# Kernel optimization log

Hardware: AMD Instinct MI355X
Metric: run time of the kernel (lower is better)

The kernel has to match this reference:

```python
import jax, jax.numpy as jnp
import numpy as np

N = 20480      # total nodes
E = 327680     # total edges (avg degree 16)
B = 16         # graphs in batch
IN = 16        # node feature dim
H = 8          # hidden_out_channel
CO = 64        # conv_out_channel
ET = 36        # n_edge_types
EF = 2         # edge_features
OUT = 1        # classifier out
DIMS = [(IN, H), (H, H), (H, H), (H, CO)]


def setup_inputs() -> dict:
    key = jax.random.key(0)
    ks = jax.random.split(key, 32)
    inp = {}
    inp['x'] = jax.random.normal(ks[0], (N, IN), jnp.float32)
    inp['edge_index'] = jax.random.randint(ks[1], (2, E), 0, N)
    inp['edge_type'] = jax.random.randint(ks[2], (E,), 0, ET)
    inp['edge_attr'] = jax.random.normal(ks[3], (E, EF), jnp.float32)
    inp['cell_type'] = jax.random.randint(ks[4], (N,), 0, 2)
    inp['batch'] = (jnp.arange(N) // (N // B)).astype(jnp.int32)
    i = 5
    for l, (ci, co) in enumerate(DIMS, 1):
        d = ci * co
        s = 1.0 / np.sqrt(EF)
        inp[f'emb{l}'] = jax.random.normal(ks[i], (ET, d), jnp.float32) * 0.02; i += 1
        inp[f'wh{l}'] = jax.random.normal(ks[i], (EF, d), jnp.float32) * s; i += 1
        inp[f'bh{l}'] = jnp.zeros((d,), jnp.float32)
        inp[f'wg{l}'] = jax.random.normal(ks[i], (EF, d), jnp.float32) * s; i += 1
        inp[f'bg{l}'] = jnp.zeros((d,), jnp.float32)
        inp[f'root{l}'] = jax.random.normal(ks[i], (ci, co), jnp.float32) / np.sqrt(ci); i += 1
        inp[f'bias{l}'] = jnp.zeros((co,), jnp.float32)
    inp['clf_w'] = jax.random.normal(ks[i], (CO, OUT), jnp.float32) / np.sqrt(CO)
    inp['clf_b'] = jnp.zeros((OUT,), jnp.float32)
    return inp


def edge_weights(etype, ef, emb, wh, bh, wg, bg):
    # EdgeNN: relu(embedding(type) * fc_h(feat) + fc_g(feat)) -> [E, cin*cout]
    return jax.nn.relu(emb[etype] * (ef @ wh + bh) + (ef @ wg + bg))


def nnconv(h, src, dst, W, root, bias):
    # NNConv(aggr='mean', root_weight=True): gather src feats, per-edge matmul, scatter-mean
    cin, cout = root.shape
    msg = jnp.einsum('ei,eio->eo', h[src], W.reshape(-1, cin, cout))  # [E, cout]
    agg = jax.ops.segment_sum(msg, dst, num_segments=N)
    deg = jax.ops.segment_sum(jnp.ones_like(msg[:, 0]), dst, num_segments=N)
    return agg / jnp.maximum(deg, 1.0)[:, None] + h @ root + bias


def reference(x, edge_index, edge_type, edge_attr, cell_type, batch,
              emb1, wh1, bh1, wg1, bg1, root1, bias1,
              emb2, wh2, bh2, wg2, bg2, root2, bias2,
              emb3, wh3, bh3, wg3, bg3, root3, bias3,
              emb4, wh4, bh4, wg4, bg4, root4, bias4,
              clf_w, clf_b):
    src, dst = edge_index[0], edge_index[1]
    layers = [(emb1, wh1, bh1, wg1, bg1, root1, bias1),
              (emb2, wh2, bh2, wg2, bg2, root2, bias2),
              (emb3, wh3, bh3, wg3, bg3, root3, bias3),
              (emb4, wh4, bh4, wg4, bg4, root4, bias4)]
    h = x
    for (emb, wh, bh, wg, bg, root, bias) in layers:  # fixed 4 structurally-distinct layers
        W = edge_weights(edge_type, edge_attr, emb, wh, bh, wg, bg)
        h = jax.nn.relu(nnconv(h, src, dst, W, root, bias))
    # gated scatter-mean pooling over tumor cells (cell_type == 1)
    gate = (cell_type == 1).astype(jnp.int32)
    seg = gate * (batch.astype(jnp.int32) + 1)  # 0 = masked-out bucket
    pooled = jax.ops.segment_sum(h, seg, num_segments=B + 1)
    cnt = jax.ops.segment_sum(jnp.ones((h.shape[0],), h.dtype), seg, num_segments=B + 1)
    pooled = (pooled / jnp.maximum(cnt, 1.0)[:, None])[1:B + 1]  # [B, CO]
    return jax.nn.sigmoid(pooled @ clf_w + clf_b)  # hazards [B, OUT]
```

## Files before the change

### kernel.cpp

```cpp
#include <hip/hip_runtime.h>
#include <math.h>

#define NN 20480
#define NE 327680
#define NBATCH 16

typedef float v2f __attribute__((ext_vector_type(2)));

#if __has_builtin(__builtin_elementwise_max)
#define VMAX0(a) __builtin_elementwise_max((a), (v2f){0.f, 0.f})
#else
static __device__ __forceinline__ v2f VMAX0(v2f a) {
  v2f r; r.x = fmaxf(a.x, 0.f); r.y = fmaxf(a.y, 0.f); return r;
}
#endif

__global__ void hist_kernel(const int* __restrict__ dst, int* __restrict__ cnt) {
  int e = blockIdx.x * blockDim.x + threadIdx.x;
  if (e < NE) atomicAdd(&cnt[dst[e]], 1);
}

__global__ __launch_bounds__(1024) void scan_kernel(const int* __restrict__ cnt,
                                                    int* __restrict__ off,
                                                    int* __restrict__ cur) {
  __shared__ int part[1024];
  int tid = threadIdx.x;
  const int PT = NN / 1024;
  int loc[PT];
  int run = 0;
  int base = tid * PT;
#pragma unroll
  for (int k = 0; k < PT; k++) { loc[k] = run; run += cnt[base + k]; }
  part[tid] = run;
  __syncthreads();
  for (int d = 1; d < 1024; d <<= 1) {
    int t = (tid >= d) ? part[tid - d] : 0;
    __syncthreads();
    part[tid] += t;
    __syncthreads();
  }
  int pre = (tid == 0) ? 0 : part[tid - 1];
#pragma unroll
  for (int k = 0; k < PT; k++) {
    off[base + k] = pre + loc[k];
    cur[base + k] = pre + loc[k];
  }
  if (tid == 1023) off[NN] = pre + run;
}

__global__ void scatter_kernel(const int* __restrict__ src, const int* __restrict__ dst,
                               const int* __restrict__ etype, const float* __restrict__ eattr,
                               int* __restrict__ cur, float4* __restrict__ es) {
  int e = blockIdx.x * blockDim.x + threadIdx.x;
  if (e >= NE) return;
  int d = dst[e];
  int pos = atomicAdd(&cur[d], 1);
  es[pos] = make_float4(__int_as_float(src[e]), __int_as_float(etype[e]),
                        eattr[2 * e], eattr[2 * e + 1]);
}

__global__ __launch_bounds__(256) void layer_small16(
    const int* __restrict__ off, const float4* __restrict__ es,
    const float* __restrict__ h_in,
    const float* __restrict__ emb, const float* __restrict__ wh,
    const float* __restrict__ bh, const float* __restrict__ wg,
    const float* __restrict__ bg,
    const float* __restrict__ root, const float* __restrict__ bias,
    float* __restrict__ h_out) {
  constexpr int D = 128;
  constexpr int S = D + 1;
  __shared__ float semb[36 * S];
  for (int idx = threadIdx.x; idx < 36 * D; idx += 256) {
    int t = idx / D, io = idx - t * D;
    semb[t * S + io] = emb[idx];
  }
  int lane = threadIdx.x & 63;
  int o = lane & 7;
  int ihalf = (lane >> 3) & 1;
  int esub = lane >> 4;
  int ibase = ihalf * 8;
  v2f rwh0[4], rwh1[4], rbh[4], rwg0[4], rwg1[4], rbg[4], rroot[4];
#pragma unroll
  for (int p = 0; p < 4; p++) {
    int a = (ibase + 2 * p) * 8 + o, b = (ibase + 2 * p + 1) * 8 + o;
    rwh0[p] = (v2f){wh[a], wh[b]};
    rwh1[p] = (v2f){wh[D + a], wh[D + b]};
    rbh[p]  = (v2f){bh[a], bh[b]};
    rwg0[p] = (v2f){wg[a], wg[b]};
    rwg1[p] = (v2f){wg[D + a], wg[D + b]};
    rbg[p]  = (v2f){bg[a], bg[b]};
    rroot[p] = (v2f){root[a], root[b]};
  }
  float rbias = bias[o];
  __syncthreads();
  int wid = __builtin_amdgcn_readfirstlane(blockIdx.x * 4 + (threadIdx.x >> 6));
  for (int k = 0; k < 2; k++) {
    int n = wid * 2 + k;
    int beg = off[n], end = off[n + 1];
    float acc = 0.f;
    for (int j = beg + esub; j < end; j += 4) {
      float4 rec = es[j];
      int s = __float_as_int(rec.x);
      int t = __float_as_int(rec.y);
      v2f ef0 = (v2f){rec.z, rec.z}, ef1 = (v2f){rec.w, rec.w};
      const float4* hp = (const float4*)(h_in + s * 16 + ibase);
      float4 h0 = hp[0], h1 = hp[1];
      v2f hv[4] = {(v2f){h0.x, h0.y}, (v2f){h0.z, h0.w},
                   (v2f){h1.x, h1.y}, (v2f){h1.z, h1.w}};
      const float* st = &semb[t * S + ibase * 8 + o];
      v2f msg = {0.f, 0.f};
#pragma unroll
      for (int p = 0; p < 4; p++) {
        v2f hval = ef0 * rwh0[p] + ef1 * rwh1[p] + rbh[p];
        v2f gval = ef0 * rwg0[p] + ef1 * rwg1[p] + rbg[p];
        v2f stv = (v2f){st[(2 * p) * 8], st[(2 * p + 1) * 8]};
        msg += hv[p] * VMAX0(stv * hval + gval);
      }
      acc += msg.x + msg.y;
    }
    acc += __shfl_xor(acc, 8);
    acc += __shfl_xor(acc, 16);
    acc += __shfl_xor(acc, 32);
    const float* hn = h_in + n * 16 + ibase;
    v2f rtv = {0.f, 0.f};
#pragma unroll
    for (int p = 0; p < 4; p++)
      rtv += (v2f){hn[2 * p], hn[2 * p + 1]} * rroot[p];
    float rt = rtv.x + rtv.y;
    rt += __shfl_xor(rt, 8);
    float deg = (float)(end - beg);
    float val = fmaxf(rbias + rt + acc / fmaxf(deg, 1.f), 0.f);
    if (lane < 8) h_out[n * 8 + o] = val;
  }
}

__global__ __launch_bounds__(256) void layer_small8(
    const int* __restrict__ off, const float4* __restrict__ es,
    const float* __restrict__ h_in,
    const float* __restrict__ emb, const float* __restrict__ wh,
    const float* __restrict__ bh, const float* __restrict__ wg,
    const float* __restrict__ bg,
    const float* __restrict__ root, const float* __restrict__ bias,
    float* __restrict__ h_out) {
  constexpr int D = 64;
  constexpr int S = D + 1;
  __shared__ float semb[36 * S];
  for (int idx = threadIdx.x; idx < 36 * D; idx += 256) {
    int t = idx / D, io = idx - t * D;
    semb[t * S + io] = emb[idx];
  }
  int lane = threadIdx.x & 63;
  int o = lane & 7, esub = lane >> 3;
  v2f rwh0[4], rwh1[4], rbh[4], rwg0[4], rwg1[4], rbg[4], rroot[4];
#pragma unroll
  for (int p = 0; p < 4; p++) {
    int a = (2 * p) * 8 + o, b = (2 * p + 1) * 8 + o;
    rwh0[p] = (v2f){wh[a], wh[b]};
    rwh1[p] = (v2f){wh[D + a], wh[D + b]};
    rbh[p]  = (v2f){bh[a], bh[b]};
    rwg0[p] = (v2f){wg[a], wg[b]};
    rwg1[p] = (v2f){wg[D + a], wg[D + b]};
    rbg[p]  = (v2f){bg[a], bg[b]};
    rroot[p] = (v2f){root[a], root[b]};
  }
  float rbias = bias[o];
  __syncthreads();
  int wid = __builtin_amdgcn_readfirstlane(blockIdx.x * 4 + (threadIdx.x >> 6));
  for (int k = 0; k < 4; k++) {
    int n = wid * 4 + k;
    int beg = off[n], end = off[n + 1];
    float acc = 0.f;
    for (int j = beg + esub; j < end; j += 8) {
      float4 rec = es[j];
      int s = __float_as_int(rec.x);
      int t = __float_as_int(rec.y);
      v2f ef0 = (v2f){rec.z, rec.z}, ef1 = (v2f){rec.w, rec.w};
      const float4* hp = (const float4*)(h_in + s * 8);
      float4 h0 = hp[0], h1 = hp[1];
      v2f hv[4] = {(v2f){h0.x, h0.y}, (v2f){h0.z, h0.w},
                   (v2f){h1.x, h1.y}, (v2f){h1.z, h1.w}};
      const float* st = &semb[t * S + o];
      v2f msg = {0.f, 0.f};
#pragma unroll
      for (int p = 0; p < 4; p++) {
        v2f hval = ef0 * rwh0[p] + ef1 * rwh1[p] + rbh[p];
        v2f gval = ef0 * rwg0[p] + ef1 * rwg1[p] + rbg[p];
        v2f stv = (v2f){st[(2 * p) * 8], st[(2 * p + 1) * 8]};
        msg += hv[p] * VMAX0(stv * hval + gval);
      }
      acc += msg.x + msg.y;
    }
    acc += __shfl_xor(acc, 8);
    acc += __shfl_xor(acc, 16);
    acc += __shfl_xor(acc, 32);
    float deg = (float)(end - beg);
    const float* hn = h_in + n * 8;
    v2f rtv = {0.f, 0.f};
#pragma unroll
    for (int p = 0; p < 4; p++)
      rtv += (v2f){hn[2 * p], hn[2 * p + 1]} * rroot[p];
    float val = fmaxf(rbias + rtv.x + rtv.y + acc / fmaxf(deg, 1.f), 0.f);
    if (lane < 8) h_out[n * 8 + o] = val;
  }
}

__global__ __launch_bounds__(256) void layer_l4(
    const int* __restrict__ off, const float4* __restrict__ es,
    const float* __restrict__ h_in,
    const float* __restrict__ emb, const float* __restrict__ wh,
    const float* __restrict__ bh, const float* __restrict__ wg,
    const float* __restrict__ bg,
    const float* __restrict__ root, const float* __restrict__ bias,
    float* __restrict__ h_out) {
  int lane = threadIdx.x & 63;
  v2f rwh0[4], rwh1[4], rbh[4], rwg0[4], rwg1[4], rbg[4], rroot[4];
#pragma unroll
  for (int p = 0; p < 4; p++) {
    int a = (2 * p) * 64 + lane, b = (2 * p + 1) * 64 + lane;
    rwh0[p] = (v2f){wh[a], wh[b]};
    rwh1[p] = (v2f){wh[512 + a], wh[512 + b]};
    rbh[p]  = (v2f){bh[a], bh[b]};
    rwg0[p] = (v2f){wg[a], wg[b]};
    rwg1[p] = (v2f){wg[512 + a], wg[512 + b]};
    rbg[p]  = (v2f){bg[a], bg[b]};
    rroot[p] = (v2f){root[a], root[b]};
  }
  float rbias = bias[lane];
  int n = __builtin_amdgcn_readfirstlane(blockIdx.x * 4 + (threadIdx.x >> 6));
  int beg = off[n], end = off[n + 1];
  float acc0 = 0.f, acc1 = 0.f;
  int e = beg;
  for (; e + 2 <= end; e += 2) {
    float4 r0 = es[e], r1 = es[e + 1];
    int s0 = __float_as_int(r0.x), t0 = __float_as_int(r0.y);
    int s1 = __float_as_int(r1.x), t1 = __float_as_int(r1.y);
    const float4* hp0 = (const float4*)(h_in + s0 * 8);
    const float4* hp1 = (const float4*)(h_in + s1 * 8);
    float4 a0 = hp0[0], a1 = hp0[1];
    float4 b0 = hp1[0], b1 = hp1[1];
    const float* st0 = emb + t0 * 512 + lane;
    const float* st1 = emb + t1 * 512 + lane;
    v2f sv0[4], sv1[4];
#pragma unroll
    for (int p = 0; p < 4; p++) sv0[p] = (v2f){st0[(2 * p) * 64], st0[(2 * p + 1) * 64]};
#pragma unroll
    for (int p = 0; p < 4; p++) sv1[p] = (v2f){st1[(2 * p) * 64], st1[(2 * p + 1) * 64]};
    v2f hva[4] = {(v2f){a0.x, a0.y}, (v2f){a0.z, a0.w},
                  (v2f){a1.x, a1.y}, (v2f){a1.z, a1.w}};
    v2f hvb[4] = {(v2f){b0.x, b0.y}, (v2f){b0.z, b0.w},
                  (v2f){b1.x, b1.y}, (v2f){b1.z, b1.w}};
    v2f e00 = (v2f){r0.z, r0.z}, e01 = (v2f){r0.w, r0.w};
    v2f e10 = (v2f){r1.z, r1.z}, e11 = (v2f){r1.w, r1.w};
    v2f m0 = {0.f, 0.f}, m1 = {0.f, 0.f};
#pragma unroll
    for (int p = 0; p < 4; p++) {
      v2f hv0 = e00 * rwh0[p] + e01 * rwh1[p] + rbh[p];
      v2f gv0 = e00 * rwg0[p] + e01 * rwg1[p] + rbg[p];
      m0 += hva[p] * VMAX0(sv0[p] * hv0 + gv0);
      v2f hv1 = e10 * rwh0[p] + e11 * rwh1[p] + rbh[p];
      v2f gv1 = e10 * rwg0[p] + e11 * rwg1[p] + rbg[p];
      m1 += hvb[p] * VMAX0(sv1[p] * hv1 + gv1);
    }
    acc0 += m0.x + m0.y;
    acc1 += m1.x + m1.y;
  }
  if (e < end) {
    float4 r0 = es[e];
    int s0 = __float_as_int(r0.x), t0 = __float_as_int(r0.y);
    const float4* hp0 = (const float4*)(h_in + s0 * 8);
    float4 a0 = hp0[0], a1 = hp0[1];
    const float* st0 = emb + t0 * 512 + lane;
    v2f hva[4] = {(v2f){a0.x, a0.y}, (v2f){a0.z, a0.w},
                  (v2f){a1.x, a1.y}, (v2f){a1.z, a1.w}};
    v2f e00 = (v2f){r0.z, r0.z}, e01 = (v2f){r0.w, r0.w};
    v2f m0 = {0.f, 0.f};
#pragma unroll
    for (int p = 0; p < 4; p++) {
      v2f hv0 = e00 * rwh0[p] + e01 * rwh1[p] + rbh[p];
      v2f gv0 = e00 * rwg0[p] + e01 * rwg1[p] + rbg[p];
      v2f stv = (v2f){st0[(2 * p) * 64], st0[(2 * p + 1) * 64]};
      m0 += hva[p] * VMAX0(stv * hv0 + gv0);
    }
    acc0 += m0.x + m0.y;
  }
  float acc = acc0 + acc1;
  float deg = (float)(end - beg);
  const float* hn = h_in + n * 8;
  v2f rtv = {0.f, 0.f};
#pragma unroll
  for (int p = 0; p < 4; p++)
    rtv += (v2f){hn[2 * p], hn[2 * p + 1]} * rroot[p];
  h_out[n * 64 + lane] = fmaxf(rbias + rtv.x + rtv.y + acc / fmaxf(deg, 1.f), 0.f);
}

__global__ __launch_bounds__(256) void pool1_kernel(
    const float* __restrict__ h4, const int* __restrict__ ct,
    float* __restrict__ pooled, float* __restrict__ pcnt) {
  __shared__ float ss[4][64];
  __shared__ float sc[4];
  int b = blockIdx.x / 20, c = blockIdx.x % 20;
  int base = b * (NN / NBATCH) + c * 64;
  int o = threadIdx.x & 63, sub = threadIdx.x >> 6;
  float sum = 0.f, cnt = 0.f;
  for (int j = sub; j < 64; j += 4) {
    int n = base + j;
    if (ct[n] == 1) { sum += h4[n * 64 + o]; cnt += 1.f; }
  }
  ss[sub][o] = sum;
  if (o == 0) sc[sub] = cnt;
  __syncthreads();
  if (threadIdx.x < 64) {
    float tot = ss[0][o] + ss[1][o] + ss[2][o] + ss[3][o];
    unsafeAtomicAdd(&pooled[b * 64 + o], tot);
    if (o == 0) unsafeAtomicAdd(&pcnt[b], sc[0] + sc[1] + sc[2] + sc[3]);
  }
}

__global__ __launch_bounds__(1024) void pool2_kernel(
    const float* __restrict__ pooled, const float* __restrict__ pcnt,
    const float* __restrict__ clf_w, const float* __restrict__ clf_b,
    float* __restrict__ out) {
  int b = threadIdx.x >> 6, o = threadIdx.x & 63;
  float c = pcnt[b];
  float v = (pooled[b * 64 + o] / fmaxf(c, 1.f)) * clf_w[o];
#pragma unroll
  for (int d = 32; d; d >>= 1) v += __shfl_down(v, d);
  if (o == 0) out[b] = 1.f / (1.f + expf(-(v + clf_b[0])));
}

extern "C" void kernel_launch(void* const* d_in, const int* in_sizes, int n_in,
                              void* d_out, int out_size, void* d_ws, size_t ws_size,
                              hipStream_t stream) {
  (void)in_sizes; (void)n_in; (void)out_size; (void)ws_size;
  const float* x     = (const float*)d_in[0];
  const int*   eidx  = (const int*)d_in[1];
  const int*   src   = eidx;
  const int*   dst   = eidx + NE;
  const int*   etype = (const int*)d_in[2];
  const float* eattr = (const float*)d_in[3];
  const int*   ct    = (const int*)d_in[4];
  const float *emb[4], *wh[4], *bh[4], *wg[4], *bg[4], *root[4], *bias[4];
  for (int l = 0; l < 4; l++) {
    int b0 = 6 + 7 * l;
    emb[l]  = (const float*)d_in[b0 + 0];
    wh[l]   = (const float*)d_in[b0 + 1];
    bh[l]   = (const float*)d_in[b0 + 2];
    wg[l]   = (const float*)d_in[b0 + 3];
    bg[l]   = (const float*)d_in[b0 + 4];
    root[l] = (const float*)d_in[b0 + 5];
    bias[l] = (const float*)d_in[b0 + 6];
  }
  const float* clf_w = (const float*)d_in[34];
  const float* clf_b = (const float*)d_in[35];
  float* outp = (float*)d_out;

  float* ws  = (float*)d_ws;
  int*    off    = (int*)ws;
  float4* es     = (float4*)(ws + 20484);
  float*  hA     = ws + 20484 + 4 * NE;
  float*  hB     = hA + 8 * NN;
  float*  h4     = hB + 8 * NN;
  float*  pooled = h4 + 64 * NN;
  float*  pcnt   = pooled + 16 * 64;
  int*    cnt    = (int*)h4;
  int*    cur    = cnt + NN;

  hipMemsetAsync(cnt, 0, NN * sizeof(int), stream);
  hipMemsetAsync(pooled, 0, (16 * 64 + 16) * sizeof(float), stream);
  hist_kernel<<<NE / 256, 256, 0, stream>>>(dst, cnt);
  scan_kernel<<<1, 1024, 0, stream>>>(cnt, off, cur);
  scatter_kernel<<<NE / 256, 256, 0, stream>>>(src, dst, etype, eattr, cur, es);

  layer_small16<<<2560, 256, 0, stream>>>(off, es, x,
      emb[0], wh[0], bh[0], wg[0], bg[0], root[0], bias[0], hA);
  layer_small8<<<1280, 256, 0, stream>>>(off, es, hA,
      emb[1], wh[1], bh[1], wg[1], bg[1], root[1], bias[1], hB);
  layer_small8<<<1280, 256, 0, stream>>>(off, es, hB,
      emb[2], wh[2], bh[2], wg[2], bg[2], root[2], bias[2], hA);
  layer_l4<<<5120, 256, 0, stream>>>(off, es, hA,
      emb[3], wh[3], bh[3], wg[3], bg[3], root[3], bias[3], h4);

  pool1_kernel<<<320, 256, 0, stream>>>(h4, ct, pooled, pcnt);
  pool2_kernel<<<1, 1024, 0, stream>>>(pooled, pcnt, clf_w, clf_b, outp);
}
```

Before: 298.6 us.

## Pre-transpose edge-type embeddings and drop shared-memory staging in layer kernels

Adds a transpose kernel that reorders each layer's edge-type embedding table so a lane's per-output weights are contiguous, allowing float4 global loads instead of strided scalar reads. The small layers no longer stage the embedding into shared memory or sync, process one node per wave, and software-pipeline the next edge record and source features. The aim is to remove per-block LDS fill cost and strided loads. The trade-off is an extra kernel launch, more blocks, and reliance on cache for embedding reuse.

```diff
diff --git a/kernel.cpp b/kernel.cpp
--- a/kernel.cpp
+++ b/kernel.cpp
@@ -59,21 +59,35 @@
                         eattr[2 * e], eattr[2 * e + 1]);
 }
 
+__global__ __launch_bounds__(256) void transpose_kernel(
+    const float* __restrict__ e1, const float* __restrict__ e2,
+    const float* __restrict__ e3, const float* __restrict__ e4,
+    float* __restrict__ t1, float* __restrict__ t2,
+    float* __restrict__ t3, float* __restrict__ t4) {
+  int idx = blockIdx.x * 256 + threadIdx.x;
+  if (idx < 36 * 128) {
+    int t = idx >> 7, r = idx & 127, o = r >> 4, i = r & 15;
+    t1[idx] = e1[(t << 7) + i * 8 + o];
+  }
+  if (idx < 36 * 64) {
+    int t = idx >> 6, r = idx & 63, o = r >> 3, i = r & 7;
+    t2[idx] = e2[(t << 6) + i * 8 + o];
+    t3[idx] = e3[(t << 6) + i * 8 + o];
+  }
+  {
+    int t = idx >> 9, r = idx & 511, o = r >> 3, i = r & 7;
+    t4[idx] = e4[(t << 9) + i * 64 + o];
+  }
+}
+
 __global__ __launch_bounds__(256) void layer_small16(
     const int* __restrict__ off, const float4* __restrict__ es,
-    const float* __restrict__ h_in,
-    const float* __restrict__ emb, const float* __restrict__ wh,
-    const float* __restrict__ bh, const float* __restrict__ wg,
-    const float* __restrict__ bg,
+    const float* __restrict__ h_in, const float* __restrict__ embT,
+    const float* __restrict__ wh, const float* __restrict__ bh,
+    const float* __restrict__ wg, const float* __restrict__ bg,
     const float* __restrict__ root, const float* __restrict__ bias,
     float* __restrict__ h_out) {
   constexpr int D = 128;
-  constexpr int S = D + 1;
-  __shared__ float semb[36 * S];
-  for (int idx = threadIdx.x; idx < 36 * D; idx += 256) {
-    int t = idx / D, io = idx - t * D;
-    semb[t * S + io] = emb[idx];
-  }
   int lane = threadIdx.x & 63;
   int o = lane & 7;
   int ihalf = (lane >> 3) & 1;
@@ -92,63 +106,63 @@
     rroot[p] = (v2f){root[a], root[b]};
   }
   float rbias = bias[o];
-  __syncthreads();
-  int wid = __builtin_amdgcn_readfirstlane(blockIdx.x * 4 + (threadIdx.x >> 6));
-  for (int k = 0; k < 2; k++) {
-    int n = wid * 2 + k;
-    int beg = off[n], end = off[n + 1];
-    float acc = 0.f;
-    for (int j = beg + esub; j < end; j += 4) {
-      float4 rec = es[j];
-      int s = __float_as_int(rec.x);
-      int t = __float_as_int(rec.y);
-      v2f ef0 = (v2f){rec.z, rec.z}, ef1 = (v2f){rec.w, rec.w};
-      const float4* hp = (const float4*)(h_in + s * 16 + ibase);
-      float4 h0 = hp[0], h1 = hp[1];
-      v2f hv[4] = {(v2f){h0.x, h0.y}, (v2f){h0.z, h0.w},
-                   (v2f){h1.x, h1.y}, (v2f){h1.z, h1.w}};
-      const float* st = &semb[t * S + ibase * 8 + o];
-      v2f msg = {0.f, 0.f};
-#pragma unroll
-      for (int p = 0; p < 4; p++) {
-        v2f hval = ef0 * rwh0[p] + ef1 * rwh1[p] + rbh[p];
-        v2f gval = ef0 * rwg0[p] + ef1 * rwg1[p] + rbg[p];
-        v2f stv = (v2f){st[(2 * p) * 8], st[(2 * p + 1) * 8]};
-        msg += hv[p] * VMAX0(stv * hval + gval);
-      }
-      acc += msg.x + msg.y;
+  int n = __builtin_amdgcn_readfirstlane((int)(blockIdx.x * 4) + (int)(threadIdx.x >> 6));
+  int beg = off[n], end = off[n + 1];
+  int nIter = (end - beg + 3) >> 2;
+  float acc = 0.f;
+  int j = beg + esub;
+  bool val0 = j < end;
+  float4 rec0 = val0 ? es[j] : make_float4(0.f, 0.f, 0.f, 0.f);
+  int s0 = __float_as_int(rec0.x);
+  const float4* hp0 = (const float4*)(h_in + s0 * 16 + ibase);
+  float4 hA0 = hp0[0], hB0 = hp0[1];
+  for (int it = 0; it < nIter; ++it) {
+    int j1 = j + 4;
+    bool val1 = j1 < end;
+    float4 rec1 = val1 ? es[j1] : make_float4(0.f, 0.f, 0.f, 0.f);
+    int s1 = __float_as_int(rec1.x);
+    const float4* hp1 = (const float4*)(h_in + s1 * 16 + ibase);
+    float4 hA1 = hp1[0], hB1 = hp1[1];
+    int t0 = __float_as_int(rec0.y);
+    const float4* sp = (const float4*)(embT + t0 * 128 + o * 16 + ibase);
+    float4 sv0 = sp[0], sv1 = sp[1];
+    v2f stv[4] = {(v2f){sv0.x, sv0.y}, (v2f){sv0.z, sv0.w},
+                  (v2f){sv1.x, sv1.y}, (v2f){sv1.z, sv1.w}};
+    v2f hv[4] = {(v2f){hA0.x, hA0.y}, (v2f){hA0.z, hA0.w},
+                 (v2f){hB0.x, hB0.y}, (v2f){hB0.z, hB0.w}};
+    v2f ef0 = (v2f){rec0.z, rec0.z}, ef1 = (v2f){rec0.w, rec0.w};
+    v2f msg = {0.f, 0.f};
+#pragma unroll
+    for (int p = 0; p < 4; p++) {
+      v2f hval = ef0 * rwh0[p] + ef1 * rwh1[p] + rbh[p];
+      v2f gval = ef0 * rwg0[p] + ef1 * rwg1[p] + rbg[p];
+      msg += hv[p] * VMAX0(stv[p] * hval + gval);
     }
-    acc += __shfl_xor(acc, 8);
-    acc += __shfl_xor(acc, 16);
-    acc += __shfl_xor(acc, 32);
-    const float* hn = h_in + n * 16 + ibase;
-    v2f rtv = {0.f, 0.f};
-#pragma unroll
-    for (int p = 0; p < 4; p++)
-      rtv += (v2f){hn[2 * p], hn[2 * p + 1]} * rroot[p];
-    float rt = rtv.x + rtv.y;
-    rt += __shfl_xor(rt, 8);
-    float deg = (float)(end - beg);
-    float val = fmaxf(rbias + rt + acc / fmaxf(deg, 1.f), 0.f);
-    if (lane < 8) h_out[n * 8 + o] = val;
-  }
+    acc += val0 ? (msg.x + msg.y) : 0.f;
+    rec0 = rec1; hA0 = hA1; hB0 = hB1; val0 = val1; j = j1;
+  }
+  acc += __shfl_xor(acc, 8);
+  acc += __shfl_xor(acc, 16);
+  acc += __shfl_xor(acc, 32);
+  const float* hn = h_in + n * 16 + ibase;
+  v2f rtv = {0.f, 0.f};
+#pragma unroll
+  for (int p = 0; p < 4; p++)
+    rtv += (v2f){hn[2 * p], hn[2 * p + 1]} * rroot[p];
+  float rt = rtv.x + rtv.y;
+  rt += __shfl_xor(rt, 8);
+  float deg = (float)(end - beg);
+  float val = fmaxf(rbias + rt + acc / fmaxf(deg, 1.f), 0.f);
+  if (lane < 8) h_out[n * 8 + o] = val;
 }
 
 __global__ __launch_bounds__(256) void layer_small8(
     const int* __restrict__ off, const float4* __restrict__ es,
-    const float* __restrict__ h_in,
-    const float* __restrict__ emb, const float* __restrict__ wh,
-    const float* __restrict__ bh, const float* __restrict__ wg,
-    const float* __restrict__ bg,
+    const float* __restrict__ h_in, const float* __restrict__ embT,
+    const float* __restrict__ wh, const float* __restrict__ bh,
+    const float* __restrict__ wg, const float* __restrict__ bg,
     const float* __restrict__ root, const float* __restrict__ bias,
     float* __restrict__ h_out) {
-  constexpr int D = 64;
-  constexpr int S = D + 1;
-  __shared__ float semb[36 * S];
-  for (int idx = threadIdx.x; idx < 36 * D; idx += 256) {
-    int t = idx / D, io = idx - t * D;
-    semb[t * S + io] = emb[idx];
-  }
   int lane = threadIdx.x & 63;
   int o = lane & 7, esub = lane >> 3;
   v2f rwh0[4], rwh1[4], rbh[4], rwg0[4], rwg1[4], rbg[4], rroot[4];
@@ -156,60 +170,67 @@
   for (int p = 0; p < 4; p++) {
     int a = (2 * p) * 8 + o, b = (2 * p + 1) * 8 + o;
     rwh0[p] = (v2f){wh[a], wh[b]};
-    rwh1[p] = (v2f){wh[D + a], wh[D + b]};
+    rwh1[p] = (v2f){wh[64 + a], wh[64 + b]};
     rbh[p]  = (v2f){bh[a], bh[b]};
     rwg0[p] = (v2f){wg[a], wg[b]};
-    rwg1[p] = (v2f){wg[D + a], wg[D + b]};
+    rwg1[p] = (v2f){wg[64 + a], wg[64 + b]};
     rbg[p]  = (v2f){bg[a], bg[b]};
     rroot[p] = (v2f){root[a], root[b]};
   }
   float rbias = bias[o];
-  __syncthreads();
-  int wid = __builtin_amdgcn_readfirstlane(blockIdx.x * 4 + (threadIdx.x >> 6));
-  for (int k = 0; k < 4; k++) {
-    int n = wid * 4 + k;
-    int beg = off[n], end = off[n + 1];
-    float acc = 0.f;
-    for (int j = beg + esub; j < end; j += 8) {
-      float4 rec = es[j];
-      int s = __float_as_int(rec.x);
-      int t = __float_as_int(rec.y);
-      v2f ef0 = (v2f){rec.z, rec.z}, ef1 = (v2f){rec.w, rec.w};
-      const float4* hp = (const float4*)(h_in + s * 8);
-      float4 h0 = hp[0], h1 = hp[1];
-      v2f hv[4] = {(v2f){h0.x, h0.y}, (v2f){h0.z, h0.w},
-                   (v2f){h1.x, h1.y}, (v2f){h1.z, h1.w}};
-      const float* st = &semb[t * S + o];
-      v2f msg = {0.f, 0.f};
-#pragma unroll
-      for (int p = 0; p < 4; p++) {
-        v2f hval = ef0 * rwh0[p] + ef1 * rwh1[p] + rbh[p];
-        v2f gval = ef0 * rwg0[p] + ef1 * rwg1[p] + rbg[p];
-        v2f stv = (v2f){st[(2 * p) * 8], st[(2 * p + 1) * 8]};
-        msg += hv[p] * VMAX0(stv * hval + gval);
-      }
-      acc += msg.x + msg.y;
+  int n = __builtin_amdgcn_readfirstlane((int)(blockIdx.x * 4) + (int)(threadIdx.x >> 6));
+  int beg = off[n], end = off[n + 1];
+  int nIter = (end - beg + 7) >> 3;
+  float acc = 0.f;
+  int j = beg + esub;
+  bool val0 = j < end;
+  float4 rec0 = val0 ? es[j] : make_float4(0.f, 0.f, 0.f, 0.f);
+  int s0 = __float_as_int(rec0.x);
+  const float4* hp0 = (const float4*)(h_in + s0 * 8);
+  float4 hA0 = hp0[0], hB0 = hp0[1];
+  for (int it = 0; it < nIter; ++it) {
+    int j1 = j + 8;
+    bool val1 = j1 < end;
+    float4 rec1 = val1 ? es[j1] : make_float4(0.f, 0.f, 0.f, 0.f);
+    int s1 = __float_as_int(rec1.x);
+    const float4* hp1 = (const float4*)(h_in + s1 * 8);
+    float4 hA1 = hp1[0], hB1 = hp1[1];
+    int t0 = __float_as_int(rec0.y);
+    const float4* sp = (const float4*)(embT + t0 * 64 + o * 8);
+    float4 sv0 = sp[0], sv1 = sp[1];
+    v2f stv[4] = {(v2f){sv0.x, sv0.y}, (v2f){sv0.z, sv0.w},
+                  (v2f){sv1.x, sv1.y}, (v2f){sv1.z, sv1.w}};
+    v2f hv[4] = {(v2f){hA0.x, hA0.y}, (v2f){hA0.z, hA0.w},
+                 (v2f){hB0.x, hB0.y}, (v2f){hB0.z, hB0.w}};
+    v2f ef0 = (v2f){rec0.z, rec0.z}, ef1 = (v2f){rec0.w, rec0.w};
+    v2f msg = {0.f, 0.f};
+#pragma unroll
+    for (int p = 0; p < 4; p++) {
+      v2f hval = ef0 * rwh0[p] + ef1 * rwh1[p] + rbh[p];
+      v2f gval = ef0 * rwg0[p] + ef1 * rwg1[p] + rbg[p];
+      msg += hv[p] * VMAX0(stv[p] * hval + gval);
     }
-    acc += __shfl_xor(acc, 8);
-    acc += __shfl_xor(acc, 16);
-    acc += __shfl_xor(acc, 32);
-    float deg = (float)(end - beg);
-    const float* hn = h_in + n * 8;
-    v2f rtv = {0.f, 0.f};
-#pragma unroll
-    for (int p = 0; p < 4; p++)
-      rtv += (v2f){hn[2 * p], hn[2 * p + 1]} * rroot[p];
-    float val = fmaxf(rbias + rtv.x + rtv.y + acc / fmaxf(deg, 1.f), 0.f);
-    if (lane < 8) h_out[n * 8 + o] = val;
-  }
+    acc += val0 ? (msg.x + msg.y) : 0.f;
+    rec0 = rec1; hA0 = hA1; hB0 = hB1; val0 = val1; j = j1;
+  }
+  acc += __shfl_xor(acc, 8);
+  acc += __shfl_xor(acc, 16);
+  acc += __shfl_xor(acc, 32);
+  const float* hn = h_in + n * 8;
+  v2f rtv = {0.f, 0.f};
+#pragma unroll
+  for (int p = 0; p < 4; p++)
+    rtv += (v2f){hn[2 * p], hn[2 * p + 1]} * rroot[p];
+  float deg = (float)(end - beg);
+  float val = fmaxf(rbias + rtv.x + rtv.y + acc / fmaxf(deg, 1.f), 0.f);
+  if (lane < 8) h_out[n * 8 + o] = val;
 }
 
 __global__ __launch_bounds__(256) void layer_l4(
     const int* __restrict__ off, const float4* __restrict__ es,
-    const float* __restrict__ h_in,
-    const float* __restrict__ emb, const float* __restrict__ wh,
-    const float* __restrict__ bh, const float* __restrict__ wg,
-    const float* __restrict__ bg,
+    const float* __restrict__ h_in, const float* __restrict__ embT,
+    const float* __restrict__ wh, const float* __restrict__ bh,
+    const float* __restrict__ wg, const float* __restrict__ bg,
     const float* __restrict__ root, const float* __restrict__ bias,
     float* __restrict__ h_out) {
   int lane = threadIdx.x & 63;
@@ -226,7 +247,7 @@
     rroot[p] = (v2f){root[a], root[b]};
   }
   float rbias = bias[lane];
-  int n = __builtin_amdgcn_readfirstlane(blockIdx.x * 4 + (threadIdx.x >> 6));
+  int n = __builtin_amdgcn_readfirstlane((int)(blockIdx.x * 4) + (int)(threadIdx.x >> 6));
   int beg = off[n], end = off[n + 1];
   float acc0 = 0.f, acc1 = 0.f;
   int e = beg;
@@ -238,13 +259,14 @@
     const float4* hp1 = (const float4*)(h_in + s1 * 8);
     float4 a0 = hp0[0], a1 = hp0[1];
     float4 b0 = hp1[0], b1 = hp1[1];
-    const float* st0 = emb + t0 * 512 + lane;
-    const float* st1 = emb + t1 * 512 + lane;
-    v2f sv0[4], sv1[4];
-#pragma unroll
-    for (int p = 0; p < 4; p++) sv0[p] = (v2f){st0[(2 * p) * 64], st0[(2 * p + 1) * 64]};
-#pragma unroll
-    for (int p = 0; p < 4; p++) sv1[p] = (v2f){st1[(2 * p) * 64], st1[(2 * p + 1) * 64]};
+    const float4* ep0 = (const float4*)(embT + t0 * 512 + lane * 8);
+    const float4* ep1 = (const float4*)(embT + t1 * 512 + lane * 8);
+    float4 s00 = ep0[0], s01 = ep0[1];
+    float4 s10 = ep1[0], s11 = ep1[1];
+    v2f sv0[4] = {(v2f){s00.x, s00.y}, (v2f){s00.z, s00.w},
+                  (v2f){s01.x, s01.y}, (v2f){s01.z, s01.w}};
+    v2f sv1[4] = {(v2f){s10.x, s10.y}, (v2f){s10.z, s10.w},
+                  (v2f){s11.x, s11.y}, (v2f){s11.z, s11.w}};
     v2f hva[4] = {(v2f){a0.x, a0.y}, (v2f){a0.z, a0.w},
                   (v2f){a1.x, a1.y}, (v2f){a1.z, a1.w}};
     v2f hvb[4] = {(v2f){b0.x, b0.y}, (v2f){b0.z, b0.w},
@@ -269,7 +291,10 @@
     int s0 = __float_as_int(r0.x), t0 = __float_as_int(r0.y);
     const float4* hp0 = (const float4*)(h_in + s0 * 8);
     float4 a0 = hp0[0], a1 = hp0[1];
-    const float* st0 = emb + t0 * 512 + lane;
+    const float4* ep0 = (const float4*)(embT + t0 * 512 + lane * 8);
+    float4 s00 = ep0[0], s01 = ep0[1];
+    v2f sv0[4] = {(v2f){s00.x, s00.y}, (v2f){s00.z, s00.w},
+                  (v2f){s01.x, s01.y}, (v2f){s01.z, s01.w}};
     v2f hva[4] = {(v2f){a0.x, a0.y}, (v2f){a0.z, a0.w},
                   (v2f){a1.x, a1.y}, (v2f){a1.z, a1.w}};
     v2f e00 = (v2f){r0.z, r0.z}, e01 = (v2f){r0.w, r0.w};
@@ -278,8 +303,7 @@
     for (int p = 0; p < 4; p++) {
       v2f hv0 = e00 * rwh0[p] + e01 * rwh1[p] + rbh[p];
       v2f gv0 = e00 * rwg0[p] + e01 * rwg1[p] + rbg[p];
-      v2f stv = (v2f){st0[(2 * p) * 64], st0[(2 * p + 1) * 64]};
-      m0 += hva[p] * VMAX0(stv * hv0 + gv0);
+      m0 += hva[p] * VMAX0(sv0[p] * hv0 + gv0);
     }
     acc0 += m0.x + m0.y;
   }
@@ -360,7 +384,11 @@
   float*  hA     = ws + 20484 + 4 * NE;
   float*  hB     = hA + 8 * NN;
   float*  h4     = hB + 8 * NN;
-  float*  pooled = h4 + 64 * NN;
+  float*  embT1  = h4 + 64 * NN;
+  float*  embT2  = embT1 + 36 * 128;
+  float*  embT3  = embT2 + 36 * 64;
+  float*  embT4  = embT3 + 36 * 64;
+  float*  pooled = embT4 + 36 * 512;
   float*  pcnt   = pooled + 16 * 64;
   int*    cnt    = (int*)h4;
   int*    cur    = cnt + NN;
@@ -368,17 +396,19 @@
   hipMemsetAsync(cnt, 0, NN * sizeof(int), stream);
   hipMemsetAsync(pooled, 0, (16 * 64 + 16) * sizeof(float), stream);
   hist_kernel<<<NE / 256, 256, 0, stream>>>(dst, cnt);
+  transpose_kernel<<<72, 256, 0, stream>>>(emb[0], emb[1], emb[2], emb[3],
+                                           embT1, embT2, embT3, embT4);
   scan_kernel<<<1, 1024, 0, stream>>>(cnt, off, cur);
   scatter_kernel<<<NE / 256, 256, 0, stream>>>(src, dst, etype, eattr, cur, es);
 
-  layer_small16<<<2560, 256, 0, stream>>>(off, es, x,
-      emb[0], wh[0], bh[0], wg[0], bg[0], root[0], bias[0], hA);
-  layer_small8<<<1280, 256, 0, stream>>>(off, es, hA,
-      emb[1], wh[1], bh[1], wg[1], bg[1], root[1], bias[1], hB);
-  layer_small8<<<1280, 256, 0, stream>>>(off, es, hB,
-      emb[2], wh[2], bh[2], wg[2], bg[2], root[2], bias[2], hA);
-  layer_l4<<<5120, 256, 0, stream>>>(off, es, hA,
-      emb[3], wh[3], bh[3], wg[3], bg[3], root[3], bias[3], h4);
+  layer_small16<<<NN / 4, 256, 0, stream>>>(off, es, x, embT1,
+      wh[0], bh[0], wg[0], bg[0], root[0], bias[0], hA);
+  layer_small8<<<NN / 4, 256, 0, stream>>>(off, es, hA, embT2,
+      wh[1], bh[1], wg[1], bg[1], root[1], bias[1], hB);
+  layer_small8<<<NN / 4, 256, 0, stream>>>(off, es, hB, embT3,
+      wh[2], bh[2], wg[2], bg[2], root[2], bias[2], hA);
+  layer_l4<<<NN / 4, 256, 0, stream>>>(off, es, hA, embT4,
+      wh[3], bh[3], wg[3], bg[3], root[3], bias[3], h4);
 
   pool1_kernel<<<320, 256, 0, stream>>>(h4, ct, pooled, pcnt);
   pool2_kernel<<<1, 1024, 0, stream>>>(pooled, pcnt, clf_w, clf_b, outp);
```

New measurement: 305.4 us. +2.3%, slower.

## Transpose layer-4 edge embedding for vectorized loads and merge setup launches

Applied to the files above, without the earlier changes.

Adds a prep kernel that runs the destination histogram and also transposes the layer-4 embedding table, so each lane owns its 8 contiguous weights. Layer 4 then reads them with two float4 loads instead of eight strided scalar loads. The pooled-buffer memset moves into the scan kernel and the separate hist kernel is removed, which cuts launch count. The cost is a small extra transpose pass and a different per-lane assignment of columns in the embedding gather.

```diff
diff --git a/kernel.cpp b/kernel.cpp
--- a/kernel.cpp
+++ b/kernel.cpp
@@ -7,24 +7,32 @@
 
 typedef float v2f __attribute__((ext_vector_type(2)));
 
-#if __has_builtin(__builtin_elementwise_max)
-#define VMAX0(a) __builtin_elementwise_max((a), (v2f){0.f, 0.f})
-#else
-static __device__ __forceinline__ v2f VMAX0(v2f a) {
+static __device__ __forceinline__ v2f vmax0(v2f a) {
   v2f r; r.x = fmaxf(a.x, 0.f); r.y = fmaxf(a.y, 0.f); return r;
 }
-#endif
-
-__global__ void hist_kernel(const int* __restrict__ dst, int* __restrict__ cnt) {
-  int e = blockIdx.x * blockDim.x + threadIdx.x;
-  if (e < NE) atomicAdd(&cnt[dst[e]], 1);
+#define VMAX0 vmax0
+
+__global__ __launch_bounds__(256) void prep_kernel(
+    const int* __restrict__ dst, int* __restrict__ cnt,
+    const float* __restrict__ e4, float* __restrict__ t4) {
+  int b = blockIdx.x;
+  if (b < NE / 256) {
+    int e = b * 256 + threadIdx.x;
+    atomicAdd(&cnt[dst[e]], 1);
+  } else {
+    int idx = (b - NE / 256) * 256 + threadIdx.x;
+    int t = idx >> 9, r = idx & 511, o = r >> 3, i = r & 7;
+    t4[idx] = e4[(t << 9) + i * 64 + o];
+  }
 }
 
 __global__ __launch_bounds__(1024) void scan_kernel(const int* __restrict__ cnt,
                                                     int* __restrict__ off,
-                                                    int* __restrict__ cur) {
+                                                    int* __restrict__ cur,
+                                                    float* __restrict__ poolz) {
   __shared__ int part[1024];
   int tid = threadIdx.x;
+  if (tid < NBATCH * 64 + NBATCH) poolz[tid] = 0.f;
   const int PT = NN / 1024;
   int loc[PT];
   int run = 0;
@@ -206,10 +214,9 @@
 
 __global__ __launch_bounds__(256) void layer_l4(
     const int* __restrict__ off, const float4* __restrict__ es,
-    const float* __restrict__ h_in,
-    const float* __restrict__ emb, const float* __restrict__ wh,
-    const float* __restrict__ bh, const float* __restrict__ wg,
-    const float* __restrict__ bg,
+    const float* __restrict__ h_in, const float* __restrict__ embT,
+    const float* __restrict__ wh, const float* __restrict__ bh,
+    const float* __restrict__ wg, const float* __restrict__ bg,
     const float* __restrict__ root, const float* __restrict__ bias,
     float* __restrict__ h_out) {
   int lane = threadIdx.x & 63;
@@ -226,7 +233,7 @@
     rroot[p] = (v2f){root[a], root[b]};
   }
   float rbias = bias[lane];
-  int n = __builtin_amdgcn_readfirstlane(blockIdx.x * 4 + (threadIdx.x >> 6));
+  int n = __builtin_amdgcn_readfirstlane((int)(blockIdx.x * 4) + (int)(threadIdx.x >> 6));
   int beg = off[n], end = off[n + 1];
   float acc0 = 0.f, acc1 = 0.f;
   int e = beg;
@@ -238,13 +245,14 @@
     const float4* hp1 = (const float4*)(h_in + s1 * 8);
     float4 a0 = hp0[0], a1 = hp0[1];
     float4 b0 = hp1[0], b1 = hp1[1];
-    const float* st0 = emb + t0 * 512 + lane;
-    const float* st1 = emb + t1 * 512 + lane;
-    v2f sv0[4], sv1[4];
-#pragma unroll
-    for (int p = 0; p < 4; p++) sv0[p] = (v2f){st0[(2 * p) * 64], st0[(2 * p + 1) * 64]};
-#pragma unroll
-    for (int p = 0; p < 4; p++) sv1[p] = (v2f){st1[(2 * p) * 64], st1[(2 * p + 1) * 64]};
+    const float4* ep0 = (const float4*)(embT + t0 * 512 + lane * 8);
+    const float4* ep1 = (const float4*)(embT + t1 * 512 + lane * 8);
+    float4 s00 = ep0[0], s01 = ep0[1];
+    float4 s10 = ep1[0], s11 = ep1[1];
+    v2f sv0[4] = {(v2f){s00.x, s00.y}, (v2f){s00.z, s00.w},
+                  (v2f){s01.x, s01.y}, (v2f){s01.z, s01.w}};
+    v2f sv1[4] = {(v2f){s10.x, s10.y}, (v2f){s10.z, s10.w},
+                  (v2f){s11.x, s11.y}, (v2f){s11.z, s11.w}};
     v2f hva[4] = {(v2f){a0.x, a0.y}, (v2f){a0.z, a0.w},
                   (v2f){a1.x, a1.y}, (v2f){a1.z, a1.w}};
     v2f hvb[4] = {(v2f){b0.x, b0.y}, (v2f){b0.z, b0.w},
@@ -269,7 +277,10 @@
     int s0 = __float_as_int(r0.x), t0 = __float_as_int(r0.y);
     const float4* hp0 = (const float4*)(h_in + s0 * 8);
     float4 a0 = hp0[0], a1 = hp0[1];
-    const float* st0 = emb + t0 * 512 + lane;
+    const float4* ep0 = (const float4*)(embT + t0 * 512 + lane * 8);
+    float4 s00 = ep0[0], s01 = ep0[1];
+    v2f sv0[4] = {(v2f){s00.x, s00.y}, (v2f){s00.z, s00.w},
+                  (v2f){s01.x, s01.y}, (v2f){s01.z, s01.w}};
     v2f hva[4] = {(v2f){a0.x, a0.y}, (v2f){a0.z, a0.w},
                   (v2f){a1.x, a1.y}, (v2f){a1.z, a1.w}};
     v2f e00 = (v2f){r0.z, r0.z}, e01 = (v2f){r0.w, r0.w};
@@ -278,8 +289,7 @@
     for (int p = 0; p < 4; p++) {
       v2f hv0 = e00 * rwh0[p] + e01 * rwh1[p] + rbh[p];
       v2f gv0 = e00 * rwg0[p] + e01 * rwg1[p] + rbg[p];
-      v2f stv = (v2f){st0[(2 * p) * 64], st0[(2 * p + 1) * 64]};
-      m0 += hva[p] * VMAX0(stv * hv0 + gv0);
+      m0 += hva[p] * VMAX0(sv0[p] * hv0 + gv0);
     }
     acc0 += m0.x + m0.y;
   }
@@ -360,15 +370,15 @@
   float*  hA     = ws + 20484 + 4 * NE;
   float*  hB     = hA + 8 * NN;
   float*  h4     = hB + 8 * NN;
-  float*  pooled = h4 + 64 * NN;
+  float*  embT4  = h4 + 64 * NN;
+  float*  pooled = embT4 + 36 * 512;
   float*  pcnt   = pooled + 16 * 64;
   int*    cnt    = (int*)h4;
   int*    cur    = cnt + NN;
 
   hipMemsetAsync(cnt, 0, NN * sizeof(int), stream);
-  hipMemsetAsync(pooled, 0, (16 * 64 + 16) * sizeof(float), stream);
-  hist_kernel<<<NE / 256, 256, 0, stream>>>(dst, cnt);
-  scan_kernel<<<1, 1024, 0, stream>>>(cnt, off, cur);
+  prep_kernel<<<NE / 256 + 72, 256, 0, stream>>>(dst, cnt, emb[3], embT4);
+  scan_kernel<<<1, 1024, 0, stream>>>(cnt, off, cur, pooled);
   scatter_kernel<<<NE / 256, 256, 0, stream>>>(src, dst, etype, eattr, cur, es);
 
   layer_small16<<<2560, 256, 0, stream>>>(off, es, x,
@@ -377,8 +387,8 @@
       emb[1], wh[1], bh[1], wg[1], bg[1], root[1], bias[1], hB);
   layer_small8<<<1280, 256, 0, stream>>>(off, es, hB,
       emb[2], wh[2], bh[2], wg[2], bg[2], root[2], bias[2], hA);
-  layer_l4<<<5120, 256, 0, stream>>>(off, es, hA,
-      emb[3], wh[3], bh[3], wg[3], bg[3], root[3], bias[3], h4);
+  layer_l4<<<NN / 4, 256, 0, stream>>>(off, es, hA, embT4,
+      wh[3], bh[3], wg[3], bg[3], root[3], bias[3], h4);
 
   pool1_kernel<<<320, 256, 0, stream>>>(h4, ct, pooled, pcnt);
   pool2_kernel<<<1, 1024, 0, stream>>>(pooled, pcnt, clf_w, clf_b, outp);
```

Result: no change. 293.5 us (-1.7%).
